# Kernel tuning notes

Measured on AMD Instinct MI355X. Metric: run time of the kernel, lower is better.

## Reference

```python
import jax, jax.numpy as jnp
import numpy as np

BJORCK_BETA = 0.5
BJORCK_ITERS = 25

def bjorck_orthonormalize(w, iters=BJORCK_ITERS):
    # Order-2 Bjorck iteration (beta must be 0.5):
    # w <- 15/8 * w - 5/4 * w (w^T w) + 3/8 * w (w^T w)^2
    def body(i, w):
        wtw = w.T @ w                     # [out, out] on the thin side
        wtw2 = wtw @ wtw
        return 1.875 * w - 1.25 * (w @ wtw) + 0.375 * (w @ wtw2)
    return jax.lax.fori_loop(0, iters, body, w)

def setup_inputs() -> dict:
    key = jax.random.key(0)
    k1, k2, k3 = jax.random.split(key, 3)
    N, D_IN, D_OUT = 8192, 512, 256
    x = jax.random.normal(k1, (N, D_IN), dtype=jnp.float32)
    adj = jax.random.uniform(k2, (N, N), dtype=jnp.float32)
    weight = jax.random.normal(k3, (D_OUT, D_IN), dtype=jnp.float32) / np.sqrt(D_IN)
    return {"x": x, "adj": adj, "weight": weight}

def reference(x, adj, weight):
    # safe Bjorck scaling: sqrt(rows * cols) of the weight (shape-only constant)
    scaling = jnp.sqrt(jnp.float32(weight.shape[0] * weight.shape[1]))
    # orthonormalize weight.T / scaling, then transpose back -> [out, in]
    ortho_w = bjorck_orthonormalize(weight.T / scaling).T
    h = x @ ortho_w.T                      # [N, out] == F.linear(x, ortho_w)
    return jax.nn.relu(adj @ h)            # [N, out]
```

## Files before the change

kernel.cpp:

```cpp
#include <hip/hip_runtime.h>

typedef __attribute__((ext_vector_type(8))) short bf16x8;
typedef __attribute__((ext_vector_type(4))) short bf16x4;
typedef __attribute__((ext_vector_type(4))) float f32x4;

__device__ __forceinline__ unsigned short f2bf(float x){
  unsigned u = __float_as_uint(x);
  u = (u + 0x7fffu + ((u >> 16) & 1u)) >> 16;
  return (unsigned short)u;
}

#define BARRIER() do { asm volatile("s_waitcnt lgkmcnt(0)" ::: "memory"); \
                       __builtin_amdgcn_s_barrier(); } while(0)

__global__ __launch_bounds__(256) void kzero(float* __restrict__ G0, float* __restrict__ n2){
  int b = blockIdx.x;
  if (b < 256) G0[b * 256 + threadIdx.x] = 0.0f;
  else if (threadIdx.x == 0) *n2 = 0.0f;
}


__global__ __launch_bounds__(256) void knorm(const float* __restrict__ wt, float* __restrict__ n2){
  int t = blockIdx.x * 256 + threadIdx.x;
  float4 v = reinterpret_cast<const float4*>(wt)[t];
  float s = v.x*v.x + v.y*v.y + v.z*v.z + v.w*v.w;
  #pragma unroll
  for (int o = 32; o > 0; o >>= 1) s += __shfl_down(s, o, 64);
  __shared__ float red[4];
  if ((threadIdx.x & 63) == 0) red[threadIdx.x >> 6] = s;
  __syncthreads();
  if (threadIdx.x == 0) atomicAdd(n2, red[0] + red[1] + red[2] + red[3]);
}

__global__ __launch_bounds__(256) void kinit(const float* __restrict__ wt, const float* __restrict__ n2,
                                             float* __restrict__ W){
  int c = blockIdx.x;
  int r = threadIdx.x;
  float s = rsqrtf(*n2) * (1.0f / 0.3f);
  W[(size_t)r * 256 + c]         = wt[(size_t)c * 512 + r] * s;
  W[(size_t)(r + 256) * 256 + c] = wt[(size_t)c * 512 + r + 256] * s;
}

__global__ __launch_bounds__(256) void kgram2(const float* __restrict__ W, float* __restrict__ G){
  __shared__ __align__(16) float Wi[64][32];
  __shared__ __align__(16) float Wj[64][32];
  const int t = threadIdx.x;
  const int i0 = blockIdx.y * 32, j0 = blockIdx.x * 32, k0 = blockIdx.z * 64;
  const int lr = t >> 3, lc = (t & 7) * 4;
  #pragma unroll
  for (int p = 0; p < 2; ++p){
    int r = lr + p * 32;
    *reinterpret_cast<float4*>(&Wi[r][lc]) =
        *reinterpret_cast<const float4*>(&W[(size_t)(k0 + r) * 256 + i0 + lc]);
    *reinterpret_cast<float4*>(&Wj[r][lc]) =
        *reinterpret_cast<const float4*>(&W[(size_t)(k0 + r) * 256 + j0 + lc]);
  }
  __syncthreads();
  const int tx = t & 31, iy = t >> 5;
  float g0 = 0, g1 = 0, g2 = 0, g3 = 0;
  #pragma unroll 8
  for (int k = 0; k < 64; ++k){
    float wj = Wj[k][tx];
    float4 wi = *reinterpret_cast<const float4*>(&Wi[k][iy * 4]);
    g0 = fmaf(wi.x, wj, g0); g1 = fmaf(wi.y, wj, g1);
    g2 = fmaf(wi.z, wj, g2); g3 = fmaf(wi.w, wj, g3);
  }
  float* gp = &G[(size_t)(i0 + iy * 4) * 256 + j0 + tx];
  atomicAdd(gp,       g0); atomicAdd(gp + 256, g1);
  atomicAdd(gp + 512, g2); atomicAdd(gp + 768, g3);
}

__global__ __launch_bounds__(512) void kupdate2(float* __restrict__ W, const float* __restrict__ G,
    float* __restrict__ Gnext, float ca, float cb, float cc, int last,
    unsigned short* __restrict__ WT2){
  __shared__ float wr[2][256], yl[2][256];
  const int t = threadIdx.x;
  const int c = t & 255, row = t >> 8;
  const int r = blockIdx.x * 2 + row;
  wr[row][c] = W[(size_t)r * 256 + c];
  __syncthreads();
  float y = 0;
  #pragma unroll 8
  for (int k = 0; k < 256; ++k)
    y = fmaf(wr[row][k], G[(size_t)k * 256 + c], y);
  yl[row][c] = y;
  __syncthreads();
  float d = 0;
  #pragma unroll 8
  for (int k = 0; k < 256; ++k)
    d = fmaf(yl[row][k], G[(size_t)k * 256 + c], d);
  float nw = ca * wr[row][c] + cb * y + cc * d;
  W[(size_t)r * 256 + c] = nw;
  if (r < 256) Gnext[(size_t)r * 256 + c] = 0.0f;
  if (last) WT2[((size_t)(r >> 3) * 256 + c) * 8 + (r & 7)] = f2bf(nw);
}


__device__ __forceinline__ bf16x8 cvtpack8(float4 a, float4 b){
  union { bf16x8 v; unsigned short u[8]; } p;
  p.u[0] = f2bf(a.x); p.u[1] = f2bf(a.y); p.u[2] = f2bf(a.z); p.u[3] = f2bf(a.w);
  p.u[4] = f2bf(b.x); p.u[5] = f2bf(b.y); p.u[6] = f2bf(b.z); p.u[7] = f2bf(b.w);
  return p.v;
}

template<int KDIM, int KS, int EPI>
__global__ __launch_bounds__(256) void kgemm3(const float* __restrict__ A,
    const unsigned short* __restrict__ B, void* __restrict__ Cout){
  __shared__ unsigned short Alds[2][4096];

  const int t = threadIdx.x;
  const int wave = t >> 6, lane = t & 63;
  const int rlo = lane & 15, l16 = lane >> 4;
  const int kp = (KS > 1) ? (blockIdx.x % KS) : 0;
  const int bm = (KS > 1) ? (blockIdx.x / KS) : blockIdx.x;
  constexpr int KLOC = KDIM / KS;
  constexpr int NS = KLOC / 64;
  const int kbase = kp * KLOC;

  const int sr = t >> 2;
  const float* aptr = A + (size_t)(bm * 64 + sr) * KDIM + kbase + (t & 3) * 16;
  const int wb0 = ((sr * 128 + (t & 3) * 32)      ) ^ ((sr & 7) << 4);
  const int wb1 = ((sr * 128 + (t & 3) * 32 + 16) ) ^ ((sr & 7) << 4);

  f32x4 acc[4][4];
  #pragma unroll
  for (int mf = 0; mf < 4; ++mf)
    #pragma unroll
    for (int nf = 0; nf < 4; ++nf){
      acc[mf][nf][0] = 0.f; acc[mf][nf][1] = 0.f; acc[mf][nf][2] = 0.f; acc[mf][nf][3] = 0.f;
    }

#define LOADA(P, s) { const float* p_ = aptr + (size_t)(s) * 64;                 \
    P[0] = *reinterpret_cast<const float4*>(p_);                                 \
    P[1] = *reinterpret_cast<const float4*>(p_ + 4);                             \
    P[2] = *reinterpret_cast<const float4*>(p_ + 8);                             \
    P[3] = *reinterpret_cast<const float4*>(p_ + 12); }
#define STOREA(buf, P) {                                                         \
    char* b_ = reinterpret_cast<char*>(&Alds[buf][0]);                           \
    *reinterpret_cast<bf16x8*>(b_ + wb0) = cvtpack8(P[0], P[1]);                 \
    *reinterpret_cast<bf16x8*>(b_ + wb1) = cvtpack8(P[2], P[3]); }

  float4 qA[4], qB[4];
  LOADA(qA, 0);
  LOADA(qB, 1);
  STOREA(0, qA);
  qA[0] = qB[0]; qA[1] = qB[1]; qA[2] = qB[2]; qA[3] = qB[3];
  LOADA(qB, 2);
  BARRIER();

  #pragma unroll 2
  for (int s = 0; s < NS; ++s){
    const int cur = s & 1;
    if (s + 1 < NS) STOREA(cur ^ 1, qA);
    bf16x8 bfr[2][4];
    #pragma unroll
    for (int ks = 0; ks < 2; ++ks)
      #pragma unroll
      for (int nf = 0; nf < 4; ++nf){
        int kb = (kbase >> 3) + s * 8 + ks * 4 + l16;
        int c  = wave * 64 + nf * 16 + rlo;
        bfr[ks][nf] = *reinterpret_cast<const bf16x8*>(B + ((size_t)kb * 256 + c) * 8);
      }
    qA[0] = qB[0]; qA[1] = qB[1]; qA[2] = qB[2]; qA[3] = qB[3];
    if (s + 3 < NS) LOADA(qB, s + 3);
    #pragma unroll
    for (int ks = 0; ks < 2; ++ks){
      bf16x8 afr[4];
      #pragma unroll
      for (int mf = 0; mf < 4; ++mf){
        int off = ((mf * 16 + rlo) * 128 + ks * 64 + l16 * 16) ^ ((rlo & 7) << 4);
        afr[mf] = *reinterpret_cast<const bf16x8*>(
            reinterpret_cast<const char*>(&Alds[cur][0]) + off);
      }
      #pragma unroll
      for (int mf = 0; mf < 4; ++mf)
        #pragma unroll
        for (int nf = 0; nf < 4; ++nf)
          acc[mf][nf] = __builtin_amdgcn_mfma_f32_16x16x32_bf16(afr[mf], bfr[ks][nf], acc[mf][nf], 0, 0, 0);
    }
    BARRIER();
  }
#undef LOADA
#undef STOREA

  if constexpr (EPI == 0){
    unsigned short* H = reinterpret_cast<unsigned short*>(Cout);
    #pragma unroll
    for (int mf = 0; mf < 4; ++mf)
      #pragma unroll
      for (int nf = 0; nf < 4; ++nf){
        int c  = wave * 64 + nf * 16 + rlo;
        int m0 = bm * 64 + mf * 16 + (l16 << 2);
        union { bf16x4 v; unsigned short u[4]; } p;
        p.u[0] = f2bf(acc[mf][nf][0]);
        p.u[1] = f2bf(acc[mf][nf][1]);
        p.u[2] = f2bf(acc[mf][nf][2]);
        p.u[3] = f2bf(acc[mf][nf][3]);
        size_t off = ((size_t)(m0 >> 3) * 256 + c) * 8 + (m0 & 7);
        *reinterpret_cast<bf16x4*>(&H[off]) = p.v;
      }
  } else {
    float* O = reinterpret_cast<float*>(Cout) + (size_t)kp * 8192 * 256;
    #pragma unroll
    for (int mf = 0; mf < 4; ++mf)
      #pragma unroll
      for (int nf = 0; nf < 4; ++nf){
        int c  = wave * 64 + nf * 16 + rlo;
        int m0 = bm * 64 + mf * 16 + (l16 << 2);
        #pragma unroll
        for (int j = 0; j < 4; ++j)
          O[(size_t)(m0 + j) * 256 + c] = acc[mf][nf][j];
      }
  }
}

__global__ __launch_bounds__(256) void kreduce8(const float* __restrict__ P, float* __restrict__ O){
  size_t i = (size_t)blockIdx.x * 256 + threadIdx.x;
  const float4* p = reinterpret_cast<const float4*>(P);
  float4 r = p[i];
  #pragma unroll
  for (int q = 1; q < 8; ++q){
    float4 b = p[i + (size_t)q * 524288];
    r.x += b.x; r.y += b.y; r.z += b.z; r.w += b.w;
  }
  r.x = fmaxf(r.x, 0.f); r.y = fmaxf(r.y, 0.f);
  r.z = fmaxf(r.z, 0.f); r.w = fmaxf(r.w, 0.f);
  reinterpret_cast<float4*>(O)[i] = r;
}


extern "C" void kernel_launch(void* const* d_in, const int* in_sizes, int n_in,
                              void* d_out, int out_size, void* d_ws, size_t ws_size,
                              hipStream_t stream) {
  const float* x   = (const float*)d_in[0];
  const float* adj = (const float*)d_in[1];
  const float* wt  = (const float*)d_in[2];
  float* out = (float*)d_out;

  char* ws = (char*)d_ws;
  float* n2            = (float*)ws;
  float* W             = (float*)(ws + 4096);
  float* G0            = (float*)(ws + 4096 + 524288);
  float* G1            = (float*)(ws + 4096 + 524288 + 262144);
  unsigned short* WT2  = (unsigned short*)(ws + 4096 + 524288 + 2*262144);
  unsigned short* HT2  = (unsigned short*)(ws + 4096 + 524288 + 3*262144);
  float* Cpart         = (float*)(ws + 4096 + 524288 + 3*262144 + 4194304);

  kzero<<<257, 256, 0, stream>>>(G0, n2);
  knorm<<<128, 256, 0, stream>>>(wt, n2);
  kinit<<<256, 256, 0, stream>>>(wt, n2, W);

  const float ca[4] = { 4.2000f, 3.4445f, 1.875f, 1.875f };
  const float cb[4] = {-9.0000f, -4.7750f, -1.25f, -1.25f };
  const float cc[4] = {-6.8000f, 2.0315f, 0.375f, 0.375f };
  float* Gb[2] = {G0, G1};
  for (int it = 0; it < 4; ++it){
    float* Gc = Gb[it & 1];
    float* Gn = Gb[(it + 1) & 1];
    kgram2<<<dim3(8, 8, 8), 256, 0, stream>>>(W, Gc);
    kupdate2<<<256, 512, 0, stream>>>(W, Gc, Gn, ca[it], cb[it], cc[it], it == 3 ? 1 : 0, WT2);
  }

  kgemm3<512, 1, 0><<<128, 256, 0, stream>>>(x, WT2, (void*)HT2);
  kgemm3<8192, 8, 1><<<1024, 256, 0, stream>>>(adj, HT2, (void*)Cpart);
  kreduce8<<<2048, 256, 0, stream>>>(Cpart, out);
}
```

Baseline: 225.4 us.

## Replace LDS-staged GEMM with register-direct A fragments and full-width waves

```diff
diff --git a/kernel.cpp b/kernel.cpp
--- a/kernel.cpp
+++ b/kernel.cpp
@@ -10,8 +10,12 @@
   return (unsigned short)u;
 }
 
-#define BARRIER() do { asm volatile("s_waitcnt lgkmcnt(0)" ::: "memory"); \
-                       __builtin_amdgcn_s_barrier(); } while(0)
+__device__ __forceinline__ bf16x8 cvtpack8(float4 a, float4 b){
+  union { bf16x8 v; unsigned short u[8]; } p;
+  p.u[0] = f2bf(a.x); p.u[1] = f2bf(a.y); p.u[2] = f2bf(a.z); p.u[3] = f2bf(a.w);
+  p.u[4] = f2bf(b.x); p.u[5] = f2bf(b.y); p.u[6] = f2bf(b.z); p.u[7] = f2bf(b.w);
+  return p.v;
+}
 
 __global__ __launch_bounds__(256) void kzero(float* __restrict__ G0, float* __restrict__ n2){
   int b = blockIdx.x;
@@ -96,101 +100,75 @@
 }
 
 
-__device__ __forceinline__ bf16x8 cvtpack8(float4 a, float4 b){
-  union { bf16x8 v; unsigned short u[8]; } p;
-  p.u[0] = f2bf(a.x); p.u[1] = f2bf(a.y); p.u[2] = f2bf(a.z); p.u[3] = f2bf(a.w);
-  p.u[4] = f2bf(b.x); p.u[5] = f2bf(b.y); p.u[6] = f2bf(b.z); p.u[7] = f2bf(b.w);
-  return p.v;
-}
-
 template<int KDIM, int KS, int EPI>
-__global__ __launch_bounds__(256) void kgemm3(const float* __restrict__ A,
+__global__ __launch_bounds__(256, 2) void kgemmW(const float* __restrict__ A,
     const unsigned short* __restrict__ B, void* __restrict__ Cout){
-  __shared__ unsigned short Alds[2][4096];
-
   const int t = threadIdx.x;
   const int wave = t >> 6, lane = t & 63;
   const int rlo = lane & 15, l16 = lane >> 4;
-  const int kp = (KS > 1) ? (blockIdx.x % KS) : 0;
-  const int bm = (KS > 1) ? (blockIdx.x / KS) : blockIdx.x;
+  const int kp = (KS > 1) ? (int)(blockIdx.x % KS) : 0;
+  const int rb = (KS > 1) ? (int)(blockIdx.x / KS) : (int)blockIdx.x;
   constexpr int KLOC = KDIM / KS;
-  constexpr int NS = KLOC / 64;
+  constexpr int NS = KLOC / 32;
   const int kbase = kp * KLOC;
 
-  const int sr = t >> 2;
-  const float* aptr = A + (size_t)(bm * 64 + sr) * KDIM + kbase + (t & 3) * 16;
-  const int wb0 = ((sr * 128 + (t & 3) * 32)      ) ^ ((sr & 7) << 4);
-  const int wb1 = ((sr * 128 + (t & 3) * 32 + 16) ) ^ ((sr & 7) << 4);
-
-  f32x4 acc[4][4];
-  #pragma unroll
-  for (int mf = 0; mf < 4; ++mf)
+  const int row0 = rb * 128 + wave * 32 + rlo;
+  const float* a0 = A + (size_t)row0 * KDIM + kbase + l16 * 8;
+  const float* a1 = a0 + (size_t)16 * KDIM;
+  const unsigned short* bp = B + ((size_t)((kbase >> 3) + l16) * 256 + rlo) * 8;
+
+  f32x4 acc[2][16];
+  #pragma unroll
+  for (int mf = 0; mf < 2; ++mf)
     #pragma unroll
-    for (int nf = 0; nf < 4; ++nf){
-      acc[mf][nf][0] = 0.f; acc[mf][nf][1] = 0.f; acc[mf][nf][2] = 0.f; acc[mf][nf][3] = 0.f;
+    for (int nf = 0; nf < 16; ++nf){
+      acc[mf][nf][0] = 0.f; acc[mf][nf][1] = 0.f;
+      acc[mf][nf][2] = 0.f; acc[mf][nf][3] = 0.f;
     }
 
-#define LOADA(P, s) { const float* p_ = aptr + (size_t)(s) * 64;                 \
-    P[0] = *reinterpret_cast<const float4*>(p_);                                 \
-    P[1] = *reinterpret_cast<const float4*>(p_ + 4);                             \
-    P[2] = *reinterpret_cast<const float4*>(p_ + 8);                             \
-    P[3] = *reinterpret_cast<const float4*>(p_ + 12); }
-#define STOREA(buf, P) {                                                         \
-    char* b_ = reinterpret_cast<char*>(&Alds[buf][0]);                           \
-    *reinterpret_cast<bf16x8*>(b_ + wb0) = cvtpack8(P[0], P[1]);                 \
-    *reinterpret_cast<bf16x8*>(b_ + wb1) = cvtpack8(P[2], P[3]); }
-
-  float4 qA[4], qB[4];
-  LOADA(qA, 0);
-  LOADA(qB, 1);
-  STOREA(0, qA);
-  qA[0] = qB[0]; qA[1] = qB[1]; qA[2] = qB[2]; qA[3] = qB[3];
-  LOADA(qB, 2);
-  BARRIER();
-
-  #pragma unroll 2
-  for (int s = 0; s < NS; ++s){
-    const int cur = s & 1;
-    if (s + 1 < NS) STOREA(cur ^ 1, qA);
-    bf16x8 bfr[2][4];
-    #pragma unroll
-    for (int ks = 0; ks < 2; ++ks)
-      #pragma unroll
-      for (int nf = 0; nf < 4; ++nf){
-        int kb = (kbase >> 3) + s * 8 + ks * 4 + l16;
-        int c  = wave * 64 + nf * 16 + rlo;
-        bfr[ks][nf] = *reinterpret_cast<const bf16x8*>(B + ((size_t)kb * 256 + c) * 8);
-      }
-    qA[0] = qB[0]; qA[1] = qB[1]; qA[2] = qB[2]; qA[3] = qB[3];
-    if (s + 3 < NS) LOADA(qB, s + 3);
-    #pragma unroll
-    for (int ks = 0; ks < 2; ++ks){
-      bf16x8 afr[4];
-      #pragma unroll
-      for (int mf = 0; mf < 4; ++mf){
-        int off = ((mf * 16 + rlo) * 128 + ks * 64 + l16 * 16) ^ ((rlo & 7) << 4);
-        afr[mf] = *reinterpret_cast<const bf16x8*>(
-            reinterpret_cast<const char*>(&Alds[cur][0]) + off);
-      }
-      #pragma unroll
-      for (int mf = 0; mf < 4; ++mf)
-        #pragma unroll
-        for (int nf = 0; nf < 4; ++nf)
-          acc[mf][nf] = __builtin_amdgcn_mfma_f32_16x16x32_bf16(afr[mf], bfr[ks][nf], acc[mf][nf], 0, 0, 0);
-    }
-    BARRIER();
-  }
-#undef LOADA
-#undef STOREA
+#define LDA(BUF, S) {                                                     \
+    BUF[0][0] = *reinterpret_cast<const float4*>(a0 + (size_t)(S) * 32);      \
+    BUF[0][1] = *reinterpret_cast<const float4*>(a0 + (size_t)(S) * 32 + 4);  \
+    BUF[1][0] = *reinterpret_cast<const float4*>(a1 + (size_t)(S) * 32);      \
+    BUF[1][1] = *reinterpret_cast<const float4*>(a1 + (size_t)(S) * 32 + 4); }
+#define LDB(BF, S) {                                                      \
+    _Pragma("unroll")                                                     \
+    for (int nf = 0; nf < 16; ++nf)                                       \
+      BF[nf] = *reinterpret_cast<const bf16x8*>(                          \
+          bp + ((size_t)(S) * 4 * 256 + nf * 16) * 8); }
+#define FMAS(BUF, BF) {                                                   \
+    bf16x8 fr0 = cvtpack8(BUF[0][0], BUF[0][1]);                          \
+    bf16x8 fr1 = cvtpack8(BUF[1][0], BUF[1][1]);                          \
+    _Pragma("unroll")                                                     \
+    for (int nf = 0; nf < 16; ++nf){                                      \
+      acc[0][nf] = __builtin_amdgcn_mfma_f32_16x16x32_bf16(fr0, BF[nf], acc[0][nf], 0, 0, 0); \
+      acc[1][nf] = __builtin_amdgcn_mfma_f32_16x16x32_bf16(fr1, BF[nf], acc[1][nf], 0, 0, 0); \
+    } }
+
+  float4 bufA[2][2], bufB[2][2];
+  LDA(bufA, 0);
+  for (int s = 0; s < NS; s += 2){
+    bf16x8 bfrA[16];
+    LDB(bfrA, s);
+    LDA(bufB, s + 1);
+    FMAS(bufA, bfrA);
+    bf16x8 bfrB[16];
+    LDB(bfrB, s + 1);
+    if (s + 2 < NS) LDA(bufA, s + 2);
+    FMAS(bufB, bfrB);
+  }
+#undef LDA
+#undef LDB
+#undef FMAS
 
   if constexpr (EPI == 0){
     unsigned short* H = reinterpret_cast<unsigned short*>(Cout);
     #pragma unroll
-    for (int mf = 0; mf < 4; ++mf)
+    for (int mf = 0; mf < 2; ++mf)
       #pragma unroll
-      for (int nf = 0; nf < 4; ++nf){
-        int c  = wave * 64 + nf * 16 + rlo;
-        int m0 = bm * 64 + mf * 16 + (l16 << 2);
+      for (int nf = 0; nf < 16; ++nf){
+        int c  = nf * 16 + rlo;
+        int m0 = rb * 128 + wave * 32 + mf * 16 + (l16 << 2);
         union { bf16x4 v; unsigned short u[4]; } p;
         p.u[0] = f2bf(acc[mf][nf][0]);
         p.u[1] = f2bf(acc[mf][nf][1]);
@@ -202,11 +180,11 @@
   } else {
     float* O = reinterpret_cast<float*>(Cout) + (size_t)kp * 8192 * 256;
     #pragma unroll
-    for (int mf = 0; mf < 4; ++mf)
+    for (int mf = 0; mf < 2; ++mf)
       #pragma unroll
-      for (int nf = 0; nf < 4; ++nf){
-        int c  = wave * 64 + nf * 16 + rlo;
-        int m0 = bm * 64 + mf * 16 + (l16 << 2);
+      for (int nf = 0; nf < 16; ++nf){
+        int c  = nf * 16 + rlo;
+        int m0 = rb * 128 + wave * 32 + mf * 16 + (l16 << 2);
         #pragma unroll
         for (int j = 0; j < 4; ++j)
           O[(size_t)(m0 + j) * 256 + c] = acc[mf][nf][j];
@@ -261,7 +239,7 @@
     kupdate2<<<256, 512, 0, stream>>>(W, Gc, Gn, ca[it], cb[it], cc[it], it == 3 ? 1 : 0, WT2);
   }
 
-  kgemm3<512, 1, 0><<<128, 256, 0, stream>>>(x, WT2, (void*)HT2);
-  kgemm3<8192, 8, 1><<<1024, 256, 0, stream>>>(adj, HT2, (void*)Cpart);
+  kgemmW<512, 1, 0><<<64, 256, 0, stream>>>(x, WT2, (void*)HT2);
+  kgemmW<8192, 8, 1><<<512, 256, 0, stream>>>(adj, HT2, (void*)Cpart);
   kreduce8<<<2048, 256, 0, stream>>>(Cpart, out);
 }
```

Result: slower. 279.4 us (+24.0%).
